# Kernel optimization log

Hardware: AMD Instinct MI355X
Metric: run time of the kernel (lower is better)

Reference implementation:

```python
import jax, jax.numpy as jnp
import numpy as np

HIDDEN = 2048
NUM_HEADS = 16
HEAD_DIM = HIDDEN // NUM_HEADS
INIT_RANGE = 0.02


def setup_inputs() -> dict:
    key = jax.random.key(0)
    ks = jax.random.split(key, 5)
    B, S = 2, 2048
    hidden_states = jax.random.normal(ks[0], (B, S, HIDDEN), dtype=jnp.float32)
    # Linear weights stored torch-style [out, in]; biases zero-init per _init_weights
    def w(k):
        return INIT_RANGE * jax.random.normal(k, (HIDDEN, HIDDEN), dtype=jnp.float32)
    return {
        "hidden_states": hidden_states,
        "wq": w(ks[1]), "bq": jnp.zeros((HIDDEN,), jnp.float32),
        "wk": w(ks[2]), "bk": jnp.zeros((HIDDEN,), jnp.float32),
        "wv": w(ks[3]), "bv": jnp.zeros((HIDDEN,), jnp.float32),
        "wo": w(ks[4]), "bo": jnp.zeros((HIDDEN,), jnp.float32),
    }


def _split_heads(x):
    # [B,S,H] -> [B,nh,S,hd]
    B, S, _ = x.shape
    return x.reshape(B, S, NUM_HEADS, HEAD_DIM).transpose(0, 2, 1, 3)


def reference(hidden_states, wq, bq, wk, bk, wv, bv, wo, bo):
    B, S, H = hidden_states.shape
    scale = 1.0 / np.sqrt(HEAD_DIM).astype(np.float32)

    q = _split_heads(hidden_states @ wq.T + bq)  # [B,nh,S,hd]
    k = _split_heads(hidden_states @ wk.T + bk)
    v = _split_heads(hidden_states @ wv.T + bv)

    attn = jnp.einsum('bhqd,bhkd->bhqk', q, k) * scale  # [B,nh,S,S]
    # causal mask: -inf above diagonal, 0 on/below
    causal = jnp.where(
        jnp.tril(jnp.ones((S, S), dtype=bool)),
        jnp.float32(0.0), jnp.float32(-jnp.inf))
    attn = attn + causal
    probs = jax.nn.softmax(attn, axis=-1)
    out = jnp.einsum('bhqk,bhkd->bhqd', probs, v)  # [B,nh,S,hd]
    out = out.transpose(0, 2, 1, 3).reshape(B, S, H)  # merge heads
    return out @ wo.T + bo
```

## Files before the change

kernel.cpp:

```cpp
#include <hip/hip_runtime.h>
#include <stdint.h>

typedef unsigned short u16;
typedef __attribute__((ext_vector_type(8))) short short8;
typedef __attribute__((ext_vector_type(4))) short short4v;
typedef __attribute__((ext_vector_type(4))) float float4v;

union V8u { short8 v; short4v h[2]; u16 u[8]; unsigned w[4]; };

__device__ __forceinline__ u16 f2bf(float f) {
  unsigned u = __float_as_uint(f);
  u = u + 0x7FFFu + ((u >> 16) & 1u);
  return (u16)(u >> 16);
}
__device__ __forceinline__ float4v fzero() {
  float4v z = {0.f, 0.f, 0.f, 0.f};
  return z;
}
__device__ __forceinline__ void gl_lds16(const u16* g, u16* l) {
  __builtin_amdgcn_global_load_lds(
      (const __attribute__((address_space(1))) void*)g,
      (__attribute__((address_space(3))) void*)l, 16, 0, 0);
}

#define MFMA16(a, b, c) __builtin_amdgcn_mfma_f32_16x16x32_bf16((a), (b), (c), 0, 0, 0)

__global__ void conv5_f32_bf16(const float* __restrict__ X,
                               const float* __restrict__ w0,
                               const float* __restrict__ w1,
                               const float* __restrict__ w2,
                               u16* __restrict__ dst, long seg) {
  const int y = blockIdx.y;
  const float* s = (y < 2) ? (X + (long)y * seg)
                           : (y == 2 ? w0 : (y == 3 ? w1 : w2));
  u16* d = dst + (long)y * seg;
  const long i = ((long)blockIdx.x * 256 + threadIdx.x) * 8;
  if (i >= seg) return;
  float4 a = *(const float4*)&s[i];
  float4 b = *(const float4*)&s[i + 4];
  V8u o;
  o.u[0] = f2bf(a.x); o.u[1] = f2bf(a.y); o.u[2] = f2bf(a.z); o.u[3] = f2bf(a.w);
  o.u[4] = f2bf(b.x); o.u[5] = f2bf(b.y); o.u[6] = f2bf(b.z); o.u[7] = f2bf(b.w);
  *(short8*)&d[i] = o.v;
}

__global__ void conv_f32_bf16(const float* __restrict__ in, u16* __restrict__ out, long n) {
  const long i = ((long)blockIdx.x * 256 + threadIdx.x) * 8;
  if (i >= n) return;
  float4 a = *(const float4*)&in[i];
  float4 b = *(const float4*)&in[i + 4];
  V8u o;
  o.u[0] = f2bf(a.x); o.u[1] = f2bf(a.y); o.u[2] = f2bf(a.z); o.u[3] = f2bf(a.w);
  o.u[4] = f2bf(b.x); o.u[5] = f2bf(b.y); o.u[6] = f2bf(b.z); o.u[7] = f2bf(b.w);
  *(short8*)&out[i] = o.v;
}

template <int NREP, bool OUTF32>
__global__ __launch_bounds__(512, 2) void gemm_bal(
    const u16* __restrict__ X, const u16* __restrict__ Wb,
    const float* __restrict__ b0, const float* __restrict__ b1,
    const float* __restrict__ b2, void* __restrict__ Out,
    int K, int cpx)
{
  constexpr int NH = NREP / 2;
  __shared__ __align__(16) u16 lds[2][(2 + NREP) * 4096];

  const int t = threadIdx.x;
  const int lane = t & 63;
  const int wave = t >> 6;
  const int quad = lane >> 4, l16 = lane & 15;
  const int wm = wave >> 2, wn = wave & 3;

  const int bid = (int)blockIdx.x;
  const int swz = (bid & 7) * cpx + (bid >> 3);
  const int by = swz & 31;
  const int bx = swz >> 5;
  const long m0 = (long)by * 128;
  const long n0 = (long)bx * (64 * NREP);

  const u16* pA[2];
  #pragma unroll
  for (int l = 0; l < 2; ++l) {
    const int d = l * 8192 + t * 16;
    const int o = d ^ ((d >> 3) & 0x70);
    pA[l] = X + (m0 + (o >> 7)) * (long)K + ((o & 127) >> 1);
  }
  const u16* pB[NREP];
  #pragma unroll
  for (int s = 0; s < NREP; ++s) {
    const int d = s * 8192 + t * 16;
    const int o = d ^ ((d >> 3) & 0x70);
    pB[s] = Wb + (n0 + (o >> 7)) * (long)K + ((o & 127) >> 1);
  }

  int offk[2];
  #pragma unroll
  for (int kk = 0; kk < 2; ++kk)
    offk[kk] = l16 * 128 + ((kk * 64 + quad * 16) ^ ((l16 & 7) << 4));

  float4v acc[4][NREP];
  #pragma unroll
  for (int i = 0; i < 4; ++i)
    #pragma unroll
    for (int j = 0; j < NREP; ++j) acc[i][j] = fzero();

  auto STAGE = [&](u16* Lb, int kt_) {
    #pragma unroll
    for (int l = 0; l < 2; ++l)
      gl_lds16(pA[l] + (long)kt_ * 64, Lb + l * 4096 + t * 8);
    #pragma unroll
    for (int s = 0; s < NREP; ++s)
      gl_lds16(pB[s] + (long)kt_ * 64, Lb + 8192 + s * 4096 + t * 8);
  };

#define SB() __builtin_amdgcn_sched_barrier(0)
#define BAR() do { asm volatile("s_barrier" ::: "memory"); SB(); } while (0)

  const int NT = K >> 6;

  STAGE(&lds[0][0], 0);
  asm volatile("s_waitcnt vmcnt(0)" ::: "memory");
  BAR();

  for (int kt = 0; kt < NT; ++kt) {
    const int buf = kt & 1;
    const int nkt = (kt + 1 < NT) ? kt + 1 : NT - 1;
    const char* Ab = (const char*)&lds[buf][0] + wm * 8192;
    const char* Bb = (const char*)&lds[buf][8192] + wn * (16 * NREP) * 128;

    short8 a[4][2], b[NREP][2];

    STAGE(&lds[buf ^ 1][0], nkt);

    #pragma unroll
    for (int i = 0; i < 4; ++i)
      a[i][0] = *(const short8*)(Ab + i * 2048 + offk[0]);
    #pragma unroll
    for (int j = 0; j < NH; ++j)
      b[j][0] = *(const short8*)(Bb + j * 2048 + offk[0]);
    #pragma unroll
    for (int j = NH; j < NREP; ++j)
      b[j][0] = *(const short8*)(Bb + j * 2048 + offk[0]);
    #pragma unroll
    for (int i = 0; i < 4; ++i)
      a[i][1] = *(const short8*)(Ab + i * 2048 + offk[1]);
    SB();

    __builtin_amdgcn_s_setprio(1);
    #pragma unroll
    for (int i = 0; i < 4; ++i)
      #pragma unroll
      for (int j = 0; j < NH; ++j)
        acc[i][j] = MFMA16(a[i][0], b[j][0], acc[i][j]);
    __builtin_amdgcn_s_setprio(0);
    SB();

    #pragma unroll
    for (int j = 0; j < NH; ++j)
      b[j][1] = *(const short8*)(Bb + j * 2048 + offk[1]);
    SB();

    __builtin_amdgcn_s_setprio(1);
    #pragma unroll
    for (int i = 0; i < 4; ++i)
      #pragma unroll
      for (int j = NH; j < NREP; ++j)
        acc[i][j] = MFMA16(a[i][0], b[j][0], acc[i][j]);
    __builtin_amdgcn_s_setprio(0);
    SB();

    #pragma unroll
    for (int j = NH; j < NREP; ++j)
      b[j][1] = *(const short8*)(Bb + j * 2048 + offk[1]);
    SB();

    __builtin_amdgcn_s_setprio(1);
    #pragma unroll
    for (int i = 0; i < 4; ++i)
      #pragma unroll
      for (int j = 0; j < NH; ++j)
        acc[i][j] = MFMA16(a[i][1], b[j][1], acc[i][j]);
    __builtin_amdgcn_s_setprio(0);
    SB();

    __builtin_amdgcn_s_setprio(1);
    #pragma unroll
    for (int i = 0; i < 4; ++i)
      #pragma unroll
      for (int j = NH; j < NREP; ++j)
        acc[i][j] = MFMA16(a[i][1], b[j][1], acc[i][j]);
    __builtin_amdgcn_s_setprio(0);

    asm volatile("s_waitcnt vmcnt(0)" ::: "memory");
    BAR();
  }

#undef SB
#undef BAR

  #pragma unroll
  for (int j = 0; j < NREP; ++j) {
    const int cg = (int)n0 + wn * (16 * NREP) + j * 16 + l16;
    const int z = cg >> 11, col = cg & 2047;
    const float* Bp = (z == 0) ? b0 : (z == 1 ? b1 : b2);
    const float bvv = Bp[col];
    #pragma unroll
    for (int i = 0; i < 4; ++i) {
      const long r0 = m0 + wm * 64 + i * 16 + quad * 4;
      #pragma unroll
      for (int r = 0; r < 4; ++r) {
        const long off = (long)z * (4096L * 2048) + (r0 + r) * 2048 + col;
        const float v = acc[i][j][r] + bvv;
        if (OUTF32) ((float*)Out)[off] = v;
        else        ((u16*)Out)[off] = f2bf(v);
      }
    }
  }
}

#define S_LEN 2048
#define HID   2048
#define HD    128

__global__ __launch_bounds__(256, 2) void attn_fwd(
    const u16* __restrict__ Q, const u16* __restrict__ K,
    const u16* __restrict__ V, u16* __restrict__ Ctx)
{
  __shared__ u16 Ks[2][32 * 136];
  __shared__ unsigned Vt[2][128 * 17];
  __shared__ u16 Ps[4 * 2 * 512];

  const int t = threadIdx.x;
  const int lane = t & 63, wave = t >> 6;
  const int quad = lane >> 4, l16 = lane & 15;
  const int b = blockIdx.y >> 4, h = blockIdx.y & 15;

  const long base = (long)b * S_LEN * HID + (long)h * HD;
  const u16* Qp = Q + base;
  const u16* Kp = K + base;
  const u16* Vp = V + base;
  u16* Cp = Ctx + base;

  const int sr2 = t >> 4;
  const int sc8 = (t & 15) * 8;

  short8 onesv;
  {
    V8u ou;
    #pragma unroll
    for (int j = 0; j < 8; ++j) ou.u[j] = 0x3F80;
    onesv = ou.v;
  }
  const float SC = 0.08838834764831845f * 1.4426950408889634f;

  for (int pass = 0; pass < 2; ++pass) {
    const int qb = (pass ? (int)blockIdx.x : 15 - (int)blockIdx.x) * 128;
    const int wqb = qb + wave * 32;

    short8 qf[2][4];
    #pragma unroll
    for (int g = 0; g < 2; ++g) {
      const long qr = wqb + g * 16 + l16;
      #pragma unroll
      for (int kk = 0; kk < 4; ++kk)
        qf[g][kk] = *(const short8*)&Qp[qr * HID + kk * 32 + quad * 8];
    }

    float4v o[2][9];
    #pragma unroll
    for (int g = 0; g < 2; ++g)
      #pragma unroll
      for (int i = 0; i < 9; ++i) o[g][i] = fzero();

    short8 kr0, kr1, vv0, vv1;
    {
      const long g = (long)(2 * sr2) * HID + sc8;
      kr0 = *(const short8*)&Kp[g];
      kr1 = *(const short8*)&Kp[g + HID];
      vv0 = *(const short8*)&Vp[g];
      vv1 = *(const short8*)&Vp[g + HID];
    }
    {
      *(short8*)&Ks[0][(2 * sr2) * 136 + sc8]     = kr0;
      *(short8*)&Ks[0][(2 * sr2 + 1) * 136 + sc8] = kr1;
      V8u a, c; a.v = vv0; c.v = vv1;
      #pragma unroll
      for (int j = 0; j < 8; ++j)
        Vt[0][(sc8 + j) * 17 + sr2] = (unsigned)a.u[j] | ((unsigned)c.u[j] << 16);
    }
    __syncthreads();

    const int T = (qb + 128) >> 5;
    for (int ti = 0; ti < T; ++ti) {
      const int kv0 = ti << 5;
      const int p = ti & 1;

      const bool more = (ti + 1 < T);
      if (more) {
        const long g = (long)(kv0 + 32 + 2 * sr2) * HID + sc8;
        kr0 = *(const short8*)&Kp[g];
        kr1 = *(const short8*)&Kp[g + HID];
        vv0 = *(const short8*)&Vp[g];
        vv1 = *(const short8*)&Vp[g + HID];
      }

      if (kv0 <= wqb) {
        float4v s[2][2];
        #pragma unroll
        for (int g = 0; g < 2; ++g) { s[g][0] = fzero(); s[g][1] = fzero(); }
        #pragma unroll
        for (int ni = 0; ni < 2; ++ni)
          #pragma unroll
          for (int kk = 0; kk < 4; ++kk) {
            short8 kf = *(const short8*)&Ks[p][(ni * 16 + l16) * 136 + kk * 32 + quad * 8];
            s[0][ni] = MFMA16(qf[0][kk], kf, s[0][ni]);
            s[1][ni] = MFMA16(qf[1][kk], kf, s[1][ni]);
          }

        const int pb = wave * 1024;
        #pragma unroll
        for (int g = 0; g < 2; ++g) {
          const int qrow0 = wqb + g * 16 + quad * 4;
          #pragma unroll
          for (int r = 0; r < 4; ++r) {
            float s0 = fminf(s[g][0][r] * SC, 80.f);
            float s1 = fminf(s[g][1][r] * SC, 80.f);
            if (kv0 + l16 > qrow0 + r)      s0 = -1e30f;
            if (kv0 + 16 + l16 > qrow0 + r) s1 = -1e30f;
            Ps[pb + g * 512 + (quad * 4 + r) * 32 + l16]      = f2bf(__builtin_amdgcn_exp2f(s0));
            Ps[pb + g * 512 + (quad * 4 + r) * 32 + 16 + l16] = f2bf(__builtin_amdgcn_exp2f(s1));
          }
        }
        __threadfence_block();
        short8 pf0 = *(const short8*)&Ps[pb + l16 * 32 + quad * 8];
        short8 pf1 = *(const short8*)&Ps[pb + 512 + l16 * 32 + quad * 8];

        #pragma unroll
        for (int dt = 0; dt < 8; ++dt) {
          const unsigned* vp = &Vt[p][(dt * 16 + l16) * 17 + quad * 4];
          V8u vf;
          vf.w[0] = vp[0]; vf.w[1] = vp[1]; vf.w[2] = vp[2]; vf.w[3] = vp[3];
          o[0][dt] = MFMA16(pf0, vf.v, o[0][dt]);
          o[1][dt] = MFMA16(pf1, vf.v, o[1][dt]);
        }
        o[0][8] = MFMA16(pf0, onesv, o[0][8]);
        o[1][8] = MFMA16(pf1, onesv, o[1][8]);
      }

      if (more) {
        *(short8*)&Ks[1 - p][(2 * sr2) * 136 + sc8]     = kr0;
        *(short8*)&Ks[1 - p][(2 * sr2 + 1) * 136 + sc8] = kr1;
        V8u a, c; a.v = vv0; c.v = vv1;
        #pragma unroll
        for (int j = 0; j < 8; ++j)
          Vt[1 - p][(sc8 + j) * 17 + sr2] = (unsigned)a.u[j] | ((unsigned)c.u[j] << 16);
      }
      __syncthreads();
    }

    #pragma unroll
    for (int g = 0; g < 2; ++g)
      #pragma unroll
      for (int r = 0; r < 4; ++r) {
        const float inv = 1.0f / o[g][8][r];
        const long qr = wqb + g * 16 + quad * 4 + r;
        #pragma unroll
        for (int dt = 0; dt < 8; ++dt)
          Cp[qr * HID + dt * 16 + l16] = f2bf(o[g][dt][r] * inv);
      }
  }
}

extern "C" void kernel_launch(void* const* d_in, const int* in_sizes, int n_in,
                              void* d_out, int out_size, void* d_ws, size_t ws_size,
                              hipStream_t stream) {
  const float* X  = (const float*)d_in[0];
  const float* wq = (const float*)d_in[1];
  const float* bq = (const float*)d_in[2];
  const float* wk = (const float*)d_in[3];
  const float* bk = (const float*)d_in[4];
  const float* wv = (const float*)d_in[5];
  const float* bv = (const float*)d_in[6];
  const float* wo = (const float*)d_in[7];
  const float* bo = (const float*)d_in[8];
  float* out = (float*)d_out;

  const long HSZ = 4096L * 2048;
  const long WSZ = 2048L * 2048;
  u16* Qw = (u16*)d_ws;
  u16* Kw = Qw + HSZ;
  u16* Vw = Kw + HSZ;
  u16* Xb = Vw + HSZ;
  u16* Wb = Xb + HSZ;
  u16* W0 = Wb;

  dim3 blk(256);
  conv5_f32_bf16<<<dim3((int)(WSZ / 2048), 5), blk, 0, stream>>>(X, wq, wk, wv, Xb, WSZ);

  gemm_bal<6, false><<<dim3(512), dim3(512), 0, stream>>>(
      Xb, Wb, bq, bk, bv, Qw, 2048, 64);

  attn_fwd<<<dim3(8, 32), blk, 0, stream>>>(Qw, Kw, Vw, Qw);

  conv_f32_bf16<<<(int)(WSZ / 2048), blk, 0, stream>>>(wo, W0, WSZ);
  gemm_bal<4, true><<<dim3(256), dim3(512), 0, stream>>>(
      Qw, W0, bo, bo, bo, out, 2048, 32);
}
```

Before: 391.3 us.

## Split attention into 1024 small 2-wave blocks with interleaved causal tile order

Replaces the 256-block grid of 4-wave blocks, each handling two 128-row query tiles in balanced pairs, with 1024 blocks of 2 waves, each owning one 64-row query tile. Block indices are mapped so heavy and light causal tiles interleave in launch order. Each thread now loads four K/V rows per stage, and the K and P LDS strides change to 132 and 40. The aim is more parallelism and better load balance across CUs, at the cost of more per-block K/V reloading and fewer waves sharing each LDS tile.

```diff
diff --git a/kernel.cpp b/kernel.cpp
--- a/kernel.cpp
+++ b/kernel.cpp
@@ -222,18 +222,26 @@
 #define HID   2048
 #define HD    128
 
-__global__ __launch_bounds__(256, 2) void attn_fwd(
+__global__ __launch_bounds__(128, 2) void attn_fwd(
     const u16* __restrict__ Q, const u16* __restrict__ K,
     const u16* __restrict__ V, u16* __restrict__ Ctx)
 {
-  __shared__ u16 Ks[2][32 * 136];
+  __shared__ u16 Ks[2][32 * 132];
   __shared__ unsigned Vt[2][128 * 17];
-  __shared__ u16 Ps[4 * 2 * 512];
+  __shared__ u16 Ps[2][2][16 * 40];
 
   const int t = threadIdx.x;
   const int lane = t & 63, wave = t >> 6;
   const int quad = lane >> 4, l16 = lane & 15;
-  const int b = blockIdx.y >> 4, h = blockIdx.y & 15;
+
+  const int L = (int)blockIdx.x;
+  const int bh = L & 31;
+  const int v = L >> 5;
+  const int s8 = v & 7, k4 = v >> 3;
+  const int tt = (k4 == 0) ? s8 : (k4 == 1) ? (15 - s8)
+               : (k4 == 2) ? (16 + s8) : (31 - s8);
+  const int b = bh >> 4, h = bh & 15;
+  const int qb = tt * 64;
 
   const long base = (long)b * S_LEN * HID + (long)h * HD;
   const u16* Qp = Q + base;
@@ -243,6 +251,16 @@
 
   const int sr2 = t >> 4;
   const int sc8 = (t & 15) * 8;
+  const int wqb = qb + wave * 32;
+
+  short8 qf[2][4];
+  #pragma unroll
+  for (int g = 0; g < 2; ++g) {
+    const long qr = wqb + g * 16 + l16;
+    #pragma unroll
+    for (int kk = 0; kk < 4; ++kk)
+      qf[g][kk] = *(const short8*)&Qp[qr * HID + kk * 32 + quad * 8];
+  }
 
   short8 onesv;
   {
@@ -253,122 +271,106 @@
   }
   const float SC = 0.08838834764831845f * 1.4426950408889634f;
 
-  for (int pass = 0; pass < 2; ++pass) {
-    const int qb = (pass ? (int)blockIdx.x : 15 - (int)blockIdx.x) * 128;
-    const int wqb = qb + wave * 32;
-
-    short8 qf[2][4];
-    #pragma unroll
-    for (int g = 0; g < 2; ++g) {
-      const long qr = wqb + g * 16 + l16;
-      #pragma unroll
-      for (int kk = 0; kk < 4; ++kk)
-        qf[g][kk] = *(const short8*)&Qp[qr * HID + kk * 32 + quad * 8];
+  float4v o[2][9];
+  #pragma unroll
+  for (int g = 0; g < 2; ++g)
+    #pragma unroll
+    for (int i = 0; i < 9; ++i) o[g][i] = fzero();
+
+  short8 kr[4], vv[4];
+  auto LOADKV = [&](int row0) {
+    const long g0 = (long)(row0 + 2 * sr2) * HID + sc8;
+    kr[0] = *(const short8*)&Kp[g0];
+    kr[1] = *(const short8*)&Kp[g0 + HID];
+    kr[2] = *(const short8*)&Kp[g0 + 16 * HID];
+    kr[3] = *(const short8*)&Kp[g0 + 17 * HID];
+    vv[0] = *(const short8*)&Vp[g0];
+    vv[1] = *(const short8*)&Vp[g0 + HID];
+    vv[2] = *(const short8*)&Vp[g0 + 16 * HID];
+    vv[3] = *(const short8*)&Vp[g0 + 17 * HID];
+  };
+  auto COMMIT = [&](int p) {
+    *(short8*)&Ks[p][(2 * sr2) * 132 + sc8]      = kr[0];
+    *(short8*)&Ks[p][(2 * sr2 + 1) * 132 + sc8]  = kr[1];
+    *(short8*)&Ks[p][(2 * sr2 + 16) * 132 + sc8] = kr[2];
+    *(short8*)&Ks[p][(2 * sr2 + 17) * 132 + sc8] = kr[3];
+    V8u a0, a1, a2, a3;
+    a0.v = vv[0]; a1.v = vv[1]; a2.v = vv[2]; a3.v = vv[3];
+    #pragma unroll
+    for (int j = 0; j < 8; ++j) {
+      Vt[p][(sc8 + j) * 17 + sr2]     = (unsigned)a0.u[j] | ((unsigned)a1.u[j] << 16);
+      Vt[p][(sc8 + j) * 17 + sr2 + 8] = (unsigned)a2.u[j] | ((unsigned)a3.u[j] << 16);
     }
-
-    float4v o[2][9];
-    #pragma unroll
-    for (int g = 0; g < 2; ++g)
-      #pragma unroll
-      for (int i = 0; i < 9; ++i) o[g][i] = fzero();
-
-    short8 kr0, kr1, vv0, vv1;
-    {
-      const long g = (long)(2 * sr2) * HID + sc8;
-      kr0 = *(const short8*)&Kp[g];
-      kr1 = *(const short8*)&Kp[g + HID];
-      vv0 = *(const short8*)&Vp[g];
-      vv1 = *(const short8*)&Vp[g + HID];
+  };
+
+  LOADKV(0);
+  COMMIT(0);
+  __syncthreads();
+
+  const int T = (qb + 64) >> 5;
+  for (int ti = 0; ti < T; ++ti) {
+    const int kv0 = ti << 5;
+    const int p = ti & 1;
+
+    const bool more = (ti + 1 < T);
+    if (more) LOADKV(kv0 + 32);
+
+    if (kv0 <= wqb) {
+      float4v s[2][2];
+      #pragma unroll
+      for (int g = 0; g < 2; ++g) { s[g][0] = fzero(); s[g][1] = fzero(); }
+      #pragma unroll
+      for (int ni = 0; ni < 2; ++ni)
+        #pragma unroll
+        for (int kk = 0; kk < 4; ++kk) {
+          short8 kf = *(const short8*)&Ks[p][(ni * 16 + l16) * 132 + kk * 32 + quad * 8];
+          s[0][ni] = MFMA16(qf[0][kk], kf, s[0][ni]);
+          s[1][ni] = MFMA16(qf[1][kk], kf, s[1][ni]);
+        }
+
+      #pragma unroll
+      for (int g = 0; g < 2; ++g) {
+        const int qrow0 = wqb + g * 16 + quad * 4;
+        #pragma unroll
+        for (int r = 0; r < 4; ++r) {
+          float s0 = fminf(s[g][0][r] * SC, 80.f);
+          float s1 = fminf(s[g][1][r] * SC, 80.f);
+          if (kv0 + l16 > qrow0 + r)      s0 = -1e30f;
+          if (kv0 + 16 + l16 > qrow0 + r) s1 = -1e30f;
+          Ps[wave][g][(quad * 4 + r) * 40 + l16]      = f2bf(__builtin_amdgcn_exp2f(s0));
+          Ps[wave][g][(quad * 4 + r) * 40 + 16 + l16] = f2bf(__builtin_amdgcn_exp2f(s1));
+        }
+      }
+      __threadfence_block();
+      short8 pf0 = *(const short8*)&Ps[wave][0][l16 * 40 + quad * 8];
+      short8 pf1 = *(const short8*)&Ps[wave][1][l16 * 40 + quad * 8];
+
+      #pragma unroll
+      for (int dt = 0; dt < 8; ++dt) {
+        const unsigned* vp = &Vt[p][(dt * 16 + l16) * 17 + quad * 4];
+        V8u vf;
+        vf.w[0] = vp[0]; vf.w[1] = vp[1]; vf.w[2] = vp[2]; vf.w[3] = vp[3];
+        o[0][dt] = MFMA16(pf0, vf.v, o[0][dt]);
+        o[1][dt] = MFMA16(pf1, vf.v, o[1][dt]);
+      }
+      o[0][8] = MFMA16(pf0, onesv, o[0][8]);
+      o[1][8] = MFMA16(pf1, onesv, o[1][8]);
     }
-    {
-      *(short8*)&Ks[0][(2 * sr2) * 136 + sc8]     = kr0;
-      *(short8*)&Ks[0][(2 * sr2 + 1) * 136 + sc8] = kr1;
-      V8u a, c; a.v = vv0; c.v = vv1;
-      #pragma unroll
-      for (int j = 0; j < 8; ++j)
-        Vt[0][(sc8 + j) * 17 + sr2] = (unsigned)a.u[j] | ((unsigned)c.u[j] << 16);
+
+    if (more) COMMIT(1 - p);
+    __syncthreads();
+  }
+
+  #pragma unroll
+  for (int g = 0; g < 2; ++g)
+    #pragma unroll
+    for (int r = 0; r < 4; ++r) {
+      const float inv = 1.0f / o[g][8][r];
+      const long qr = wqb + g * 16 + quad * 4 + r;
+      #pragma unroll
+      for (int dt = 0; dt < 8; ++dt)
+        Cp[qr * HID + dt * 16 + l16] = f2bf(o[g][dt][r] * inv);
     }
-    __syncthreads();
-
-    const int T = (qb + 128) >> 5;
-    for (int ti = 0; ti < T; ++ti) {
-      const int kv0 = ti << 5;
-      const int p = ti & 1;
-
-      const bool more = (ti + 1 < T);
-      if (more) {
-        const long g = (long)(kv0 + 32 + 2 * sr2) * HID + sc8;
-        kr0 = *(const short8*)&Kp[g];
-        kr1 = *(const short8*)&Kp[g + HID];
-        vv0 = *(const short8*)&Vp[g];
-        vv1 = *(const short8*)&Vp[g + HID];
-      }
-
-      if (kv0 <= wqb) {
-        float4v s[2][2];
-        #pragma unroll
-        for (int g = 0; g < 2; ++g) { s[g][0] = fzero(); s[g][1] = fzero(); }
-        #pragma unroll
-        for (int ni = 0; ni < 2; ++ni)
-          #pragma unroll
-          for (int kk = 0; kk < 4; ++kk) {
-            short8 kf = *(const short8*)&Ks[p][(ni * 16 + l16) * 136 + kk * 32 + quad * 8];
-            s[0][ni] = MFMA16(qf[0][kk], kf, s[0][ni]);
-            s[1][ni] = MFMA16(qf[1][kk], kf, s[1][ni]);
-          }
-
-        const int pb = wave * 1024;
-        #pragma unroll
-        for (int g = 0; g < 2; ++g) {
-          const int qrow0 = wqb + g * 16 + quad * 4;
-          #pragma unroll
-          for (int r = 0; r < 4; ++r) {
-            float s0 = fminf(s[g][0][r] * SC, 80.f);
-            float s1 = fminf(s[g][1][r] * SC, 80.f);
-            if (kv0 + l16 > qrow0 + r)      s0 = -1e30f;
-            if (kv0 + 16 + l16 > qrow0 + r) s1 = -1e30f;
-            Ps[pb + g * 512 + (quad * 4 + r) * 32 + l16]      = f2bf(__builtin_amdgcn_exp2f(s0));
-            Ps[pb + g * 512 + (quad * 4 + r) * 32 + 16 + l16] = f2bf(__builtin_amdgcn_exp2f(s1));
-          }
-        }
-        __threadfence_block();
-        short8 pf0 = *(const short8*)&Ps[pb + l16 * 32 + quad * 8];
-        short8 pf1 = *(const short8*)&Ps[pb + 512 + l16 * 32 + quad * 8];
-
-        #pragma unroll
-        for (int dt = 0; dt < 8; ++dt) {
-          const unsigned* vp = &Vt[p][(dt * 16 + l16) * 17 + quad * 4];
-          V8u vf;
-          vf.w[0] = vp[0]; vf.w[1] = vp[1]; vf.w[2] = vp[2]; vf.w[3] = vp[3];
-          o[0][dt] = MFMA16(pf0, vf.v, o[0][dt]);
-          o[1][dt] = MFMA16(pf1, vf.v, o[1][dt]);
-        }
-        o[0][8] = MFMA16(pf0, onesv, o[0][8]);
-        o[1][8] = MFMA16(pf1, onesv, o[1][8]);
-      }
-
-      if (more) {
-        *(short8*)&Ks[1 - p][(2 * sr2) * 136 + sc8]     = kr0;
-        *(short8*)&Ks[1 - p][(2 * sr2 + 1) * 136 + sc8] = kr1;
-        V8u a, c; a.v = vv0; c.v = vv1;
-        #pragma unroll
-        for (int j = 0; j < 8; ++j)
-          Vt[1 - p][(sc8 + j) * 17 + sr2] = (unsigned)a.u[j] | ((unsigned)c.u[j] << 16);
-      }
-      __syncthreads();
-    }
-
-    #pragma unroll
-    for (int g = 0; g < 2; ++g)
-      #pragma unroll
-      for (int r = 0; r < 4; ++r) {
-        const float inv = 1.0f / o[g][8][r];
-        const long qr = wqb + g * 16 + quad * 4 + r;
-        #pragma unroll
-        for (int dt = 0; dt < 8; ++dt)
-          Cp[qr * HID + dt * 16 + l16] = f2bf(o[g][dt][r] * inv);
-      }
-  }
 }
 
 extern "C" void kernel_launch(void* const* d_in, const int* in_sizes, int n_in,
@@ -400,7 +402,7 @@
   gemm_bal<6, false><<<dim3(512), dim3(512), 0, stream>>>(
       Xb, Wb, bq, bk, bv, Qw, 2048, 64);
 
-  attn_fwd<<<dim3(8, 32), blk, 0, stream>>>(Qw, Kw, Vw, Qw);
+  attn_fwd<<<dim3(1024), dim3(128), 0, stream>>>(Qw, Kw, Vw, Qw);
 
   conv_f32_bf16<<<(int)(WSZ / 2048), blk, 0, stream>>>(wo, W0, WSZ);
   gemm_bal<4, true><<<dim3(256), dim3(512), 0, stream>>>(
```

Result: no change. 396.0 us (+1.2%).

## Split GEMM tile staging into halves and prefetch two k-steps ahead

Applied to the files above, without the earlier changes.

Restructures the projection GEMM main loop so global-to-LDS staging is split into an A-plus-first-half-B group and a second-half-B group. The first group is issued two k-tiles ahead into the buffer just consumed, the second one k-tile ahead. Partial vmcnt waits replace full drains, and barriers are placed between MFMA phases. The aim is to keep more memory traffic in flight and avoid stalling on vmcnt(0) each iteration, at the cost of many more s_barrier instructions per iteration and delicate LDS reuse ordering.

```diff
diff --git a/kernel.cpp b/kernel.cpp
--- a/kernel.cpp
+++ b/kernel.cpp
@@ -104,48 +104,55 @@
     #pragma unroll
     for (int j = 0; j < NREP; ++j) acc[i][j] = fzero();
 
-  auto STAGE = [&](u16* Lb, int kt_) {
+  auto STG_ABL = [&](int bs, int kt_) {
     #pragma unroll
     for (int l = 0; l < 2; ++l)
-      gl_lds16(pA[l] + (long)kt_ * 64, Lb + l * 4096 + t * 8);
-    #pragma unroll
-    for (int s = 0; s < NREP; ++s)
-      gl_lds16(pB[s] + (long)kt_ * 64, Lb + 8192 + s * 4096 + t * 8);
+      gl_lds16(pA[l] + (long)kt_ * 64, &lds[bs][l * 4096 + t * 8]);
+    #pragma unroll
+    for (int s = 0; s < NH; ++s)
+      gl_lds16(pB[s] + (long)kt_ * 64, &lds[bs][(2 + s) * 4096 + t * 8]);
   };
-
-#define SB() __builtin_amdgcn_sched_barrier(0)
-#define BAR() do { asm volatile("s_barrier" ::: "memory"); SB(); } while (0)
+  auto STG_BH = [&](int bs, int kt_) {
+    #pragma unroll
+    for (int s = NH; s < NREP; ++s)
+      gl_lds16(pB[s] + (long)kt_ * 64, &lds[bs][(2 + s) * 4096 + t * 8]);
+  };
+
+#define VMW() do { if constexpr (NREP == 6)                                    \
+      asm volatile("s_waitcnt vmcnt(8)" ::: "memory");                         \
+    else                                                                       \
+      asm volatile("s_waitcnt vmcnt(6)" ::: "memory"); } while (0)
+#define LGKM() do { asm volatile("s_waitcnt lgkmcnt(0)" ::: "memory");         \
+                    __builtin_amdgcn_sched_barrier(0); } while (0)
+#define BAR() do { asm volatile("s_barrier" ::: "memory");                     \
+                   __builtin_amdgcn_sched_barrier(0); } while (0)
 
   const int NT = K >> 6;
 
-  STAGE(&lds[0][0], 0);
-  asm volatile("s_waitcnt vmcnt(0)" ::: "memory");
+  STG_ABL(0, 0);
+  STG_BH(0, 0);
+  STG_ABL(1, 1);
+  VMW();
   BAR();
 
   for (int kt = 0; kt < NT; ++kt) {
-    const int buf = kt & 1;
-    const int nkt = (kt + 1 < NT) ? kt + 1 : NT - 1;
-    const char* Ab = (const char*)&lds[buf][0] + wm * 8192;
-    const char* Bb = (const char*)&lds[buf][8192] + wn * (16 * NREP) * 128;
+    const int cur = kt & 1, nb = cur ^ 1;
+    const int k1 = (kt + 1 < NT) ? kt + 1 : NT - 1;
+    const int k2 = (kt + 2 < NT) ? kt + 2 : NT - 1;
+    const char* Ab = (const char*)&lds[cur][0] + wm * 8192;
+    const char* Bb = (const char*)&lds[cur][2 * 4096] + wn * (16 * NREP) * 128;
 
     short8 a[4][2], b[NREP][2];
 
-    STAGE(&lds[buf ^ 1][0], nkt);
-
+    STG_BH(nb, k1);
     #pragma unroll
     for (int i = 0; i < 4; ++i)
       a[i][0] = *(const short8*)(Ab + i * 2048 + offk[0]);
     #pragma unroll
     for (int j = 0; j < NH; ++j)
       b[j][0] = *(const short8*)(Bb + j * 2048 + offk[0]);
-    #pragma unroll
-    for (int j = NH; j < NREP; ++j)
-      b[j][0] = *(const short8*)(Bb + j * 2048 + offk[0]);
-    #pragma unroll
-    for (int i = 0; i < 4; ++i)
-      a[i][1] = *(const short8*)(Ab + i * 2048 + offk[1]);
-    SB();
-
+    BAR();
+    LGKM();
     __builtin_amdgcn_s_setprio(1);
     #pragma unroll
     for (int i = 0; i < 4; ++i)
@@ -153,13 +160,14 @@
       for (int j = 0; j < NH; ++j)
         acc[i][j] = MFMA16(a[i][0], b[j][0], acc[i][j]);
     __builtin_amdgcn_s_setprio(0);
-    SB();
-
-    #pragma unroll
-    for (int j = 0; j < NH; ++j)
-      b[j][1] = *(const short8*)(Bb + j * 2048 + offk[1]);
-    SB();
-
+    VMW();
+    BAR();
+
+    #pragma unroll
+    for (int j = NH; j < NREP; ++j)
+      b[j][0] = *(const short8*)(Bb + j * 2048 + offk[0]);
+    BAR();
+    LGKM();
     __builtin_amdgcn_s_setprio(1);
     #pragma unroll
     for (int i = 0; i < 4; ++i)
@@ -167,13 +175,16 @@
       for (int j = NH; j < NREP; ++j)
         acc[i][j] = MFMA16(a[i][0], b[j][0], acc[i][j]);
     __builtin_amdgcn_s_setprio(0);
-    SB();
-
-    #pragma unroll
-    for (int j = NH; j < NREP; ++j)
+    BAR();
+
+    #pragma unroll
+    for (int i = 0; i < 4; ++i)
+      a[i][1] = *(const short8*)(Ab + i * 2048 + offk[1]);
+    #pragma unroll
+    for (int j = 0; j < NH; ++j)
       b[j][1] = *(const short8*)(Bb + j * 2048 + offk[1]);
-    SB();
-
+    BAR();
+    LGKM();
     __builtin_amdgcn_s_setprio(1);
     #pragma unroll
     for (int i = 0; i < 4; ++i)
@@ -181,8 +192,14 @@
       for (int j = 0; j < NH; ++j)
         acc[i][j] = MFMA16(a[i][1], b[j][1], acc[i][j]);
     __builtin_amdgcn_s_setprio(0);
-    SB();
-
+    BAR();
+
+    STG_ABL(cur, k2);
+    #pragma unroll
+    for (int j = NH; j < NREP; ++j)
+      b[j][1] = *(const short8*)(Bb + j * 2048 + offk[1]);
+    BAR();
+    LGKM();
     __builtin_amdgcn_s_setprio(1);
     #pragma unroll
     for (int i = 0; i < 4; ++i)
@@ -190,12 +207,13 @@
       for (int j = NH; j < NREP; ++j)
         acc[i][j] = MFMA16(a[i][1], b[j][1], acc[i][j]);
     __builtin_amdgcn_s_setprio(0);
-
-    asm volatile("s_waitcnt vmcnt(0)" ::: "memory");
-    BAR();
-  }
-
-#undef SB
+    VMW();
+    BAR();
+  }
+  asm volatile("s_waitcnt vmcnt(0)" ::: "memory");
+
+#undef VMW
+#undef LGKM
 #undef BAR
 
   #pragma unroll
```

Measured after the change: 394.4 us. No clear change (+0.8%).

## Fuse two causal query passes into one 512-thread attention block sharing K/V tiles

Applied to the files above, without the earlier changes.

The attention kernel now uses 8 waves per block, and each wave owns 16 rows from a high query block and 16 rows from the paired low query block. Both halves are processed in a single sweep over K/V tiles, so each tile is loaded once instead of once per pass. K and V staging is split between the two halves of the thread block. Once the low block's rows are fully masked, waves compute only their high-block half. The change removes duplicated K/V traffic and the serial second pass, at the cost of lower occupancy (launch bounds 512,1) and some waves idling on partial work.

```diff
diff --git a/kernel.cpp b/kernel.cpp
--- a/kernel.cpp
+++ b/kernel.cpp
@@ -222,18 +222,24 @@
 #define HID   2048
 #define HD    128
 
-__global__ __launch_bounds__(256, 2) void attn_fwd(
+__global__ __launch_bounds__(512, 1) void attn_fwd(
     const u16* __restrict__ Q, const u16* __restrict__ K,
     const u16* __restrict__ V, u16* __restrict__ Ctx)
 {
   __shared__ u16 Ks[2][32 * 136];
   __shared__ unsigned Vt[2][128 * 17];
-  __shared__ u16 Ps[4 * 2 * 512];
+  __shared__ u16 Ps[8][2][512];
 
   const int t = threadIdx.x;
   const int lane = t & 63, wave = t >> 6;
   const int quad = lane >> 4, l16 = lane & 15;
+  const int x = (int)blockIdx.x;
   const int b = blockIdx.y >> 4, h = blockIdx.y & 15;
+
+  const int hb = (15 - x) * 128;
+  const int lb = x * 128;
+  const int rg0 = hb + wave * 16;
+  const int rg1 = lb + wave * 16;
 
   const long base = (long)b * S_LEN * HID + (long)h * HD;
   const u16* Qp = Q + base;
@@ -241,8 +247,14 @@
   const u16* Vp = V + base;
   u16* Cp = Ctx + base;
 
-  const int sr2 = t >> 4;
-  const int sc8 = (t & 15) * 8;
+  short8 qf[2][4];
+  #pragma unroll
+  for (int g = 0; g < 2; ++g) {
+    const long qr = (g ? rg1 : rg0) + l16;
+    #pragma unroll
+    for (int kk = 0; kk < 4; ++kk)
+      qf[g][kk] = *(const short8*)&Qp[qr * HID + kk * 32 + quad * 8];
+  }
 
   short8 onesv;
   {
@@ -253,58 +265,51 @@
   }
   const float SC = 0.08838834764831845f * 1.4426950408889634f;
 
-  for (int pass = 0; pass < 2; ++pass) {
-    const int qb = (pass ? (int)blockIdx.x : 15 - (int)blockIdx.x) * 128;
-    const int wqb = qb + wave * 32;
-
-    short8 qf[2][4];
-    #pragma unroll
-    for (int g = 0; g < 2; ++g) {
-      const long qr = wqb + g * 16 + l16;
-      #pragma unroll
-      for (int kk = 0; kk < 4; ++kk)
-        qf[g][kk] = *(const short8*)&Qp[qr * HID + kk * 32 + quad * 8];
+  float4v o[2][9];
+  #pragma unroll
+  for (int g = 0; g < 2; ++g)
+    #pragma unroll
+    for (int i = 0; i < 9; ++i) o[g][i] = fzero();
+
+  const int st = t & 255;
+  const int sr2 = st >> 4;
+  const int sc8 = (st & 15) * 8;
+  const bool isV = t >= 256;
+  const u16* Sp = isV ? Vp : Kp;
+
+  short8 r0, r1;
+  auto LOADKV = [&](int row0) {
+    const long g0 = (long)(row0 + 2 * sr2) * HID + sc8;
+    r0 = *(const short8*)&Sp[g0];
+    r1 = *(const short8*)&Sp[g0 + HID];
+  };
+  auto COMMIT = [&](int pb) {
+    if (!isV) {
+      *(short8*)&Ks[pb][(2 * sr2) * 136 + sc8]     = r0;
+      *(short8*)&Ks[pb][(2 * sr2 + 1) * 136 + sc8] = r1;
+    } else {
+      V8u a, c; a.v = r0; c.v = r1;
+      #pragma unroll
+      for (int j = 0; j < 8; ++j)
+        Vt[pb][(sc8 + j) * 17 + sr2] = (unsigned)a.u[j] | ((unsigned)c.u[j] << 16);
     }
-
-    float4v o[2][9];
-    #pragma unroll
-    for (int g = 0; g < 2; ++g)
-      #pragma unroll
-      for (int i = 0; i < 9; ++i) o[g][i] = fzero();
-
-    short8 kr0, kr1, vv0, vv1;
-    {
-      const long g = (long)(2 * sr2) * HID + sc8;
-      kr0 = *(const short8*)&Kp[g];
-      kr1 = *(const short8*)&Kp[g + HID];
-      vv0 = *(const short8*)&Vp[g];
-      vv1 = *(const short8*)&Vp[g + HID];
-    }
-    {
-      *(short8*)&Ks[0][(2 * sr2) * 136 + sc8]     = kr0;
-      *(short8*)&Ks[0][(2 * sr2 + 1) * 136 + sc8] = kr1;
-      V8u a, c; a.v = vv0; c.v = vv1;
-      #pragma unroll
-      for (int j = 0; j < 8; ++j)
-        Vt[0][(sc8 + j) * 17 + sr2] = (unsigned)a.u[j] | ((unsigned)c.u[j] << 16);
-    }
-    __syncthreads();
-
-    const int T = (qb + 128) >> 5;
-    for (int ti = 0; ti < T; ++ti) {
-      const int kv0 = ti << 5;
-      const int p = ti & 1;
-
-      const bool more = (ti + 1 < T);
-      if (more) {
-        const long g = (long)(kv0 + 32 + 2 * sr2) * HID + sc8;
-        kr0 = *(const short8*)&Kp[g];
-        kr1 = *(const short8*)&Kp[g + HID];
-        vv0 = *(const short8*)&Vp[g];
-        vv1 = *(const short8*)&Vp[g + HID];
-      }
-
-      if (kv0 <= wqb) {
+  };
+
+  LOADKV(0);
+  COMMIT(0);
+  __syncthreads();
+
+  const int T = (hb + 128) >> 5;
+  for (int ti = 0; ti < T; ++ti) {
+    const int kv0 = ti << 5;
+    const int p = ti & 1;
+
+    const bool more = (ti + 1 < T);
+    if (more) LOADKV(kv0 + 32);
+
+    if (kv0 <= rg0) {
+      const bool act1 = kv0 <= rg1;
+      if (act1) {
         float4v s[2][2];
         #pragma unroll
         for (int g = 0; g < 2; ++g) { s[g][0] = fzero(); s[g][1] = fzero(); }
@@ -316,24 +321,22 @@
             s[0][ni] = MFMA16(qf[0][kk], kf, s[0][ni]);
             s[1][ni] = MFMA16(qf[1][kk], kf, s[1][ni]);
           }
-
-        const int pb = wave * 1024;
         #pragma unroll
         for (int g = 0; g < 2; ++g) {
-          const int qrow0 = wqb + g * 16 + quad * 4;
+          const int qrow0 = (g ? rg1 : rg0) + quad * 4;
           #pragma unroll
           for (int r = 0; r < 4; ++r) {
             float s0 = fminf(s[g][0][r] * SC, 80.f);
             float s1 = fminf(s[g][1][r] * SC, 80.f);
             if (kv0 + l16 > qrow0 + r)      s0 = -1e30f;
             if (kv0 + 16 + l16 > qrow0 + r) s1 = -1e30f;
-            Ps[pb + g * 512 + (quad * 4 + r) * 32 + l16]      = f2bf(__builtin_amdgcn_exp2f(s0));
-            Ps[pb + g * 512 + (quad * 4 + r) * 32 + 16 + l16] = f2bf(__builtin_amdgcn_exp2f(s1));
+            Ps[wave][g][(quad * 4 + r) * 32 + l16]      = f2bf(__builtin_amdgcn_exp2f(s0));
+            Ps[wave][g][(quad * 4 + r) * 32 + 16 + l16] = f2bf(__builtin_amdgcn_exp2f(s1));
           }
         }
         __threadfence_block();
-        short8 pf0 = *(const short8*)&Ps[pb + l16 * 32 + quad * 8];
-        short8 pf1 = *(const short8*)&Ps[pb + 512 + l16 * 32 + quad * 8];
+        short8 pf0 = *(const short8*)&Ps[wave][0][l16 * 32 + quad * 8];
+        short8 pf1 = *(const short8*)&Ps[wave][1][l16 * 32 + quad * 8];
 
         #pragma unroll
         for (int dt = 0; dt < 8; ++dt) {
@@ -345,30 +348,55 @@
         }
         o[0][8] = MFMA16(pf0, onesv, o[0][8]);
         o[1][8] = MFMA16(pf1, onesv, o[1][8]);
+      } else {
+        float4v s0v[2] = {fzero(), fzero()};
+        #pragma unroll
+        for (int ni = 0; ni < 2; ++ni)
+          #pragma unroll
+          for (int kk = 0; kk < 4; ++kk) {
+            short8 kf = *(const short8*)&Ks[p][(ni * 16 + l16) * 136 + kk * 32 + quad * 8];
+            s0v[ni] = MFMA16(qf[0][kk], kf, s0v[ni]);
+          }
+        {
+          const int qrow0 = rg0 + quad * 4;
+          #pragma unroll
+          for (int r = 0; r < 4; ++r) {
+            float s0 = fminf(s0v[0][r] * SC, 80.f);
+            float s1 = fminf(s0v[1][r] * SC, 80.f);
+            if (kv0 + l16 > qrow0 + r)      s0 = -1e30f;
+            if (kv0 + 16 + l16 > qrow0 + r) s1 = -1e30f;
+            Ps[wave][0][(quad * 4 + r) * 32 + l16]      = f2bf(__builtin_amdgcn_exp2f(s0));
+            Ps[wave][0][(quad * 4 + r) * 32 + 16 + l16] = f2bf(__builtin_amdgcn_exp2f(s1));
+          }
+        }
+        __threadfence_block();
+        short8 pf0 = *(const short8*)&Ps[wave][0][l16 * 32 + quad * 8];
+
+        #pragma unroll
+        for (int dt = 0; dt < 8; ++dt) {
+          const unsigned* vp = &Vt[p][(dt * 16 + l16) * 17 + quad * 4];
+          V8u vf;
+          vf.w[0] = vp[0]; vf.w[1] = vp[1]; vf.w[2] = vp[2]; vf.w[3] = vp[3];
+          o[0][dt] = MFMA16(pf0, vf.v, o[0][dt]);
+        }
+        o[0][8] = MFMA16(pf0, onesv, o[0][8]);
       }
-
-      if (more) {
-        *(short8*)&Ks[1 - p][(2 * sr2) * 136 + sc8]     = kr0;
-        *(short8*)&Ks[1 - p][(2 * sr2 + 1) * 136 + sc8] = kr1;
-        V8u a, c; a.v = vv0; c.v = vv1;
-        #pragma unroll
-        for (int j = 0; j < 8; ++j)
-          Vt[1 - p][(sc8 + j) * 17 + sr2] = (unsigned)a.u[j] | ((unsigned)c.u[j] << 16);
-      }
-      __syncthreads();
     }
 
-    #pragma unroll
-    for (int g = 0; g < 2; ++g)
-      #pragma unroll
-      for (int r = 0; r < 4; ++r) {
-        const float inv = 1.0f / o[g][8][r];
-        const long qr = wqb + g * 16 + quad * 4 + r;
-        #pragma unroll
-        for (int dt = 0; dt < 8; ++dt)
-          Cp[qr * HID + dt * 16 + l16] = f2bf(o[g][dt][r] * inv);
-      }
-  }
+    if (more) COMMIT(1 - p);
+    __syncthreads();
+  }
+
+  #pragma unroll
+  for (int g = 0; g < 2; ++g)
+    #pragma unroll
+    for (int r = 0; r < 4; ++r) {
+      const float inv = 1.0f / o[g][8][r];
+      const long qr = (g ? rg1 : rg0) + quad * 4 + r;
+      #pragma unroll
+      for (int dt = 0; dt < 8; ++dt)
+        Cp[qr * HID + dt * 16 + l16] = f2bf(o[g][dt][r] * inv);
+    }
 }
 
 extern "C" void kernel_launch(void* const* d_in, const int* in_sizes, int n_in,
@@ -400,7 +428,7 @@
   gemm_bal<6, false><<<dim3(512), dim3(512), 0, stream>>>(
       Xb, Wb, bq, bk, bv, Qw, 2048, 64);
 
-  attn_fwd<<<dim3(8, 32), blk, 0, stream>>>(Qw, Kw, Vw, Qw);
+  attn_fwd<<<dim3(8, 32), dim3(512), 0, stream>>>(Qw, Kw, Vw, Qw);
 
   conv_f32_bf16<<<(int)(WSZ / 2048), blk, 0, stream>>>(wo, W0, WSZ);
   gemm_bal<4, true><<<dim3(256), dim3(512), 0, stream>>>(
```

After: 392.6 us. No clear change (+0.3%).
